# Optimization experiments

Measured on AMD Instinct MI355X. Metric: run time of the kernel, lower is better.

The kernel has to match this reference:

```python
import jax, jax.numpy as jnp
import numpy as np

N, S, T, D = 8, 2048, 2048, 1024


def setup_inputs() -> dict:
    key0 = jax.random.key(0)
    ks = jax.random.split(key0, 6)
    scale = 1.0 / np.sqrt(D).astype(np.float32)
    query = jax.random.normal(ks[0], (N, S, D), dtype=jnp.float32)
    key = jax.random.normal(ks[1], (N, T, D), dtype=jnp.float32)
    value = jax.random.normal(ks[2], (N, T, D), dtype=jnp.float32)
    # nn.Linear(D, D, bias=False) weights, shape [out, in]
    Wq = jax.random.normal(ks[3], (D, D), dtype=jnp.float32) * scale
    Wk = jax.random.normal(ks[4], (D, D), dtype=jnp.float32) * scale
    Wv = jax.random.normal(ks[5], (D, D), dtype=jnp.float32) * scale
    # causal mask: 1 on/below diagonal, 0 above (zeros become -inf additively)
    attn_mask = jnp.tril(jnp.ones((S, T), dtype=jnp.float32))
    return {"key": key, "query": query, "value": value,
            "Wq": Wq, "Wk": Wk, "Wv": Wv, "attn_mask": attn_mask}


def reference(key, query, value, Wq, Wk, Wv, attn_mask):
    d = query.shape[-1]
    q = query @ Wq.T              # [N,S,D]
    k = key @ Wk.T                # [N,T,D]
    v = value @ Wv.T              # [N,T,D]
    scores = jnp.einsum('nsd,ntd->nst', q, k)          # [N,S,T]
    # masked_fill(mask==0, -inf) then ADD the (nonzero) mask values
    additive = jnp.where(attn_mask == 0, -jnp.inf, attn_mask)
    scores = scores + additive                          # broadcast [S,T] -> [N,S,T]
    # NOTE: torch code divides by D**(-0.5), i.e. multiplies by sqrt(D). Faithful.
    attn = jax.nn.softmax(scores * jnp.sqrt(jnp.float32(d)), axis=-1)
    return jnp.einsum('nst,ntd->nsd', attn, v)          # [N,S,D]
```

## Files before the change

kernel.cpp:

```cpp
#include <hip/hip_runtime.h>
#include <hip/hip_bf16.h>


typedef __attribute__((ext_vector_type(4))) float f32x4;
typedef __attribute__((ext_vector_type(8))) short bf16x8;
typedef __attribute__((ext_vector_type(4))) short s16x4;

#define DEVI __device__ __forceinline__

DEVI unsigned short f2bf(float x) {
  union { float f; unsigned u; } v; v.f = x;
  unsigned r = v.u + 0x7FFFu + ((v.u >> 16) & 1u);
  return (unsigned short)(r >> 16);
}
DEVI float bf2f(unsigned short b) {
  union { float f; unsigned u; } v; v.u = ((unsigned)b) << 16;
  return v.f;
}

DEVI void gload16(const void* g, void* l) {
#if __has_builtin(__builtin_amdgcn_global_load_lds)
  typedef __attribute__((address_space(1))) const unsigned int* gas_u32;
  typedef __attribute__((address_space(3))) unsigned int* las_u32;
  __builtin_amdgcn_global_load_lds(
      (gas_u32)(unsigned long long)g,
      (las_u32)(unsigned int)(unsigned long long)l, 16, 0, 0);
#else
  *(bf16x8*)l = *(const bf16x8*)g;
#endif
}

DEVI int xcd_swizzle(int bid, int nwg) {
  if (nwg & 7) return bid;
  int cpx = nwg >> 3;
  return (bid & 7) * cpx + (bid >> 3);
}

#define WAITBAR(N) asm volatile("s_waitcnt vmcnt(" #N ")\ns_barrier" ::: "memory")
#define BAR()      asm volatile("s_barrier" ::: "memory")

DEVI void stage_pair(const unsigned short* __restrict__ s0, long long rs0,
                     const unsigned short* __restrict__ s1, long long rs1,
                     short* lds, int tid) {
#pragma unroll
  for (int it = 0; it < 4; ++it) {
    int ii = it * 256 + tid;
    int r = ii >> 3;
    int c8 = (ii & 7) ^ (r & 7);
    const unsigned short* src = (c8 < 4)
        ? s0 + (long long)r * rs0 + (c8 & 3) * 8
        : s1 + (long long)r * rs1 + (c8 & 3) * 8;
    gload16(src, &lds[ii * 8]);
  }
}

constexpr int NB = 8, SS = 2048, TT = 2048, DD = 1024;
constexpr long long TILE_E = 16384;

__global__ __launch_bounds__(256) void split_hl_k(
    const float* __restrict__ in, unsigned short* __restrict__ hi,
    unsigned short* __restrict__ lo, long long n4)
{
  long long i = (long long)blockIdx.x * 256 + threadIdx.x;
  long long stride = (long long)gridDim.x * 256;
  for (; i < n4; i += stride) {
    f32x4 v = ((const f32x4*)in)[i];
    s16x4 h, l;
#pragma unroll
    for (int e = 0; e < 4; ++e) {
      unsigned short hh = f2bf(v[e]);
      h[e] = (short)hh;
      l[e] = (short)f2bf(v[e] - bf2f(hh));
    }
    ((s16x4*)hi)[i] = h;
    ((s16x4*)lo)[i] = l;
  }
}

__global__ __launch_bounds__(256) void split_h_k(
    const float* __restrict__ in, unsigned short* __restrict__ hi, long long n4)
{
  long long i = (long long)blockIdx.x * 256 + threadIdx.x;
  long long stride = (long long)gridDim.x * 256;
  for (; i < n4; i += stride) {
    f32x4 v = ((const f32x4*)in)[i];
    s16x4 h;
#pragma unroll
    for (int e = 0; e < 4; ++e) h[e] = (short)f2bf(v[e]);
    ((s16x4*)hi)[i] = h;
  }
}

__global__ __launch_bounds__(256) void tsplit_k(
    const float* __restrict__ W, unsigned short* __restrict__ Th,
    unsigned short* __restrict__ Tl)
{
  __shared__ float t[64][68];
  int bi = blockIdx.x & 15, bj = blockIdx.x >> 4;
  int tid = threadIdx.x;
  int lr = tid >> 2, lc4 = tid & 3;
#pragma unroll
  for (int q = 0; q < 4; ++q) {
    int col = (lc4 + q * 4) * 4;
    f32x4 v = *(const f32x4*)(W + (long long)(bj * 64 + lr) * DD + bi * 64 + col);
    t[lr][col] = v[0]; t[lr][col + 1] = v[1];
    t[lr][col + 2] = v[2]; t[lr][col + 3] = v[3];
  }
  __syncthreads();
  int orow = tid >> 2, ch = tid & 3;
#pragma unroll
  for (int cc = 0; cc < 2; ++cc) {
    int c0 = (ch + cc * 4) * 8;
    bf16x8 h, l;
#pragma unroll
    for (int e = 0; e < 8; ++e) {
      float v = t[c0 + e][orow];
      unsigned short hh = f2bf(v);
      h[e] = (short)hh;
      l[e] = (short)f2bf(v - bf2f(hh));
    }
    long long o = (long long)(bi * 64 + orow) * DD + bj * 64 + c0;
    *(bf16x8*)(Th + o) = h;
    *(bf16x8*)(Tl + o) = l;
  }
}

template<int NMFMA, bool SPLIT_OUT>
__global__ __launch_bounds__(256, 2) void gemm_bt(
    const unsigned short* __restrict__ Ah_g, const unsigned short* __restrict__ Al_g,
    const unsigned short* __restrict__ Bh_g, const unsigned short* __restrict__ Bl_g,
    unsigned short* __restrict__ Chi, unsigned short* __restrict__ Clo,
    int Nn, int K,
    long long aStride, long long bStride, long long cStride,
    int tilesM, int tilesN)
{
  constexpr int HALF = (NMFMA == 3) ? 16384 : 8192;
  __shared__ short lds[2 * HALF];

  int tid = threadIdx.x;
  int lane = tid & 63, wid = tid >> 6;
  int wr = wid >> 1, wc = wid & 1;
  int l15 = lane & 15, lq = lane >> 4;

  int wg = xcd_swizzle(blockIdx.x, gridDim.x);
  int tilesM2 = tilesM >> 1;
  int tilesPer = tilesM2 * tilesN;
  int b = wg / tilesPer;
  int rem = wg % tilesPer;
  int mt2 = rem / tilesN, nt = rem % tilesN;

  const unsigned short* Bgh = Bh_g + (long long)b * bStride + (long long)nt * 128 * K;
  const unsigned short* Bgl = (NMFMA == 3) ? Bl_g + (long long)b * bStride + (long long)nt * 128 * K : nullptr;

  for (int hm = 0; hm < 2; ++hm) {
    int mt = mt2 + hm * tilesM2;
    const unsigned short* Agh = Ah_g + (long long)b * aStride + (long long)mt * 128 * K;
    const unsigned short* Agl = (NMFMA == 3) ? Al_g + (long long)b * aStride + (long long)mt * 128 * K : nullptr;

    f32x4 acc[4][4];
#pragma unroll
    for (int i = 0; i < 4; ++i)
#pragma unroll
      for (int j = 0; j < 4; ++j) acc[i][j] = (f32x4){0.f, 0.f, 0.f, 0.f};

    auto stage = [&](int t, int h) {
      int k0 = t * 32;
      if constexpr (NMFMA == 3) {
        stage_pair(Agh + k0, K, Agl + k0, K, lds + h * HALF, tid);
        stage_pair(Bgh + k0, K, Bgl + k0, K, lds + h * HALF + 8192, tid);
      } else {
        stage_pair(Agh + k0, K, Bgh + k0, K, lds + h * HALF, tid);
      }
    };
    auto compute = [&](int h) {
      __builtin_amdgcn_s_setprio(1);
      if constexpr (NMFMA == 3) {
        const short* U = lds + h * HALF;
        const short* V = U + 8192;
        bf16x8 afh[4], afl[4], bfh[4], bfl[4];
#pragma unroll
        for (int i = 0; i < 4; ++i) {
          int ra = wr * 64 + i * 16 + l15;
          int sa = (ra & 7) << 4;
          afh[i] = *(const bf16x8*)(&U[((ra * 128 + lq * 16) ^ sa) >> 1]);
          afl[i] = *(const bf16x8*)(&U[((ra * 128 + 64 + lq * 16) ^ sa) >> 1]);
          int rb = wc * 64 + i * 16 + l15;
          int sb = (rb & 7) << 4;
          bfh[i] = *(const bf16x8*)(&V[((rb * 128 + lq * 16) ^ sb) >> 1]);
          bfl[i] = *(const bf16x8*)(&V[((rb * 128 + 64 + lq * 16) ^ sb) >> 1]);
        }
#pragma unroll
        for (int i = 0; i < 4; ++i)
#pragma unroll
          for (int j = 0; j < 4; ++j) {
            acc[i][j] = __builtin_amdgcn_mfma_f32_16x16x32_bf16(afh[i], bfh[j], acc[i][j], 0, 0, 0);
            acc[i][j] = __builtin_amdgcn_mfma_f32_16x16x32_bf16(afh[i], bfl[j], acc[i][j], 0, 0, 0);
            acc[i][j] = __builtin_amdgcn_mfma_f32_16x16x32_bf16(afl[i], bfh[j], acc[i][j], 0, 0, 0);
          }
      } else {
        const short* W = lds + h * HALF;
        bf16x8 af[4], bfr[4];
#pragma unroll
        for (int i = 0; i < 4; ++i) {
          int ra = wr * 64 + i * 16 + l15;
          af[i] = *(const bf16x8*)(&W[((ra * 128 + lq * 16) ^ ((ra & 7) << 4)) >> 1]);
          int rb = wc * 64 + i * 16 + l15;
          bfr[i] = *(const bf16x8*)(&W[((rb * 128 + 64 + lq * 16) ^ ((rb & 7) << 4)) >> 1]);
        }
#pragma unroll
        for (int i = 0; i < 4; ++i)
#pragma unroll
          for (int j = 0; j < 4; ++j)
            acc[i][j] = __builtin_amdgcn_mfma_f32_16x16x32_bf16(af[i], bfr[j], acc[i][j], 0, 0, 0);
      }
      __builtin_amdgcn_s_setprio(0);
    };

    int NT = K >> 5;
    stage(0, 0);
    stage(1, 1);
    for (int t = 0; t < NT; ++t) {
      if (t < NT - 1) {
        if constexpr (NMFMA == 3) WAITBAR(8); else WAITBAR(4);
      } else {
        WAITBAR(0);
      }
      compute(t & 1);
      BAR();
      if (t + 2 < NT) stage(t + 2, t & 1);
    }

    unsigned short* ch = Chi + (long long)b * cStride;
    unsigned short* cl = SPLIT_OUT ? (Clo + (long long)b * cStride) : nullptr;
#pragma unroll
    for (int i = 0; i < 4; ++i)
#pragma unroll
      for (int j = 0; j < 4; ++j)
#pragma unroll
        for (int e = 0; e < 4; ++e) {
          int row = mt * 128 + wr * 64 + i * 16 + lq * 4 + e;
          int col = nt * 128 + wc * 64 + j * 16 + l15;
          float vv = acc[i][j][e];
          unsigned short h = f2bf(vv);
          ch[(long long)row * Nn + col] = h;
          if constexpr (SPLIT_OUT) cl[(long long)row * Nn + col] = f2bf(vv - bf2f(h));
        }
    BAR();
  }
}

__global__ __launch_bounds__(256, 2) void qk_bt(
    const unsigned short* __restrict__ qh, const unsigned short* __restrict__ ql,
    const unsigned short* __restrict__ kh, const unsigned short* __restrict__ kl,
    float* __restrict__ Sg)
{
  __shared__ short lds[2 * 16384];

  int tid = threadIdx.x;
  int lane = tid & 63, wid = tid >> 6;
  int wr = wid >> 1, wc = wid & 1;
  int l15 = lane & 15, lq = lane >> 4;

  int wg = xcd_swizzle(blockIdx.x, gridDim.x);
  int b = wg / 136;
  int idx = wg % 136;
  int st = (int)((sqrtf(8.f * (float)idx + 1.f) - 1.f) * 0.5f);
  while ((st + 1) * (st + 2) / 2 <= idx) ++st;
  while (st * (st + 1) / 2 > idx) --st;
  int tt = idx - st * (st + 1) / 2;

  const unsigned short* Agh = qh + (long long)b * SS * DD + (long long)st * 128 * DD;
  const unsigned short* Agl = ql + (long long)b * SS * DD + (long long)st * 128 * DD;
  const unsigned short* Bgh = kh + (long long)b * TT * DD + (long long)tt * 128 * DD;
  const unsigned short* Bgl = kl + (long long)b * TT * DD + (long long)tt * 128 * DD;

  f32x4 acc[4][4];
#pragma unroll
  for (int i = 0; i < 4; ++i)
#pragma unroll
    for (int j = 0; j < 4; ++j) acc[i][j] = (f32x4){0.f, 0.f, 0.f, 0.f};

  auto stage = [&](int t, int h) {
    int k0 = t * 32;
    stage_pair(Agh + k0, DD, Agl + k0, DD, lds + h * 16384, tid);
    stage_pair(Bgh + k0, DD, Bgl + k0, DD, lds + h * 16384 + 8192, tid);
  };
  auto compute = [&](int h) {
    __builtin_amdgcn_s_setprio(1);
    const short* U = lds + h * 16384;
    const short* V = U + 8192;
    bf16x8 afh[4], afl[4], bfh[4], bfl[4];
#pragma unroll
    for (int i = 0; i < 4; ++i) {
      int ra = wr * 64 + i * 16 + l15;
      int sa = (ra & 7) << 4;
      afh[i] = *(const bf16x8*)(&U[((ra * 128 + lq * 16) ^ sa) >> 1]);
      afl[i] = *(const bf16x8*)(&U[((ra * 128 + 64 + lq * 16) ^ sa) >> 1]);
      int rb = wc * 64 + i * 16 + l15;
      int sb = (rb & 7) << 4;
      bfh[i] = *(const bf16x8*)(&V[((rb * 128 + lq * 16) ^ sb) >> 1]);
      bfl[i] = *(const bf16x8*)(&V[((rb * 128 + 64 + lq * 16) ^ sb) >> 1]);
    }
#pragma unroll
    for (int i = 0; i < 4; ++i)
#pragma unroll
      for (int j = 0; j < 4; ++j) {
        acc[i][j] = __builtin_amdgcn_mfma_f32_16x16x32_bf16(afh[i], bfh[j], acc[i][j], 0, 0, 0);
        acc[i][j] = __builtin_amdgcn_mfma_f32_16x16x32_bf16(afh[i], bfl[j], acc[i][j], 0, 0, 0);
        acc[i][j] = __builtin_amdgcn_mfma_f32_16x16x32_bf16(afl[i], bfh[j], acc[i][j], 0, 0, 0);
      }
    __builtin_amdgcn_s_setprio(0);
  };

  stage(0, 0);
  stage(1, 1);
  for (int t = 0; t < 32; ++t) {
    if (t < 31) WAITBAR(8); else WAITBAR(0);
    compute(t & 1);
    BAR();
    if (t + 2 < 32) stage(t + 2, t & 1);
  }

  float* Sb = Sg + ((long long)b * 136 + idx) * TILE_E;
#pragma unroll
  for (int i = 0; i < 4; ++i)
#pragma unroll
    for (int j = 0; j < 4; ++j)
#pragma unroll
      for (int e = 0; e < 4; ++e) {
        int row = wr * 64 + i * 16 + lq * 4 + e;
        int col = wc * 64 + j * 16 + l15;
        Sb[(long long)row * 128 + col] = acc[i][j][e];
      }
}

__global__ __launch_bounds__(256) void softmax_kernel(float* __restrict__ Sg)
{
  __shared__ float red[8];
  int blk = blockIdx.x;
  int b = blk >> 11, s = blk & 2047;
  int st = s >> 7, r = s & 127;
  long long tri = (long long)st * (st + 1) / 2;
  const float* tb = Sg + ((long long)b * 136 + tri) * TILE_E + (long long)r * 128;

  int tid = threadIdx.x;
  int lane = tid & 63, wid = tid >> 6;

  int c0 = tid * 8;
  int tt = c0 >> 7, cc = c0 & 127;
  bool live = (c0 <= s);
  f32x4 v0 = {0.f, 0.f, 0.f, 0.f}, v1 = {0.f, 0.f, 0.f, 0.f};
  if (live) {
    const float* seg = tb + (long long)tt * TILE_E + cc;
    v0 = *(const f32x4*)seg;
    v1 = *(const f32x4*)(seg + 4);
  }

  float m = -3.0e38f;
#pragma unroll
  for (int e = 0; e < 4; ++e) {
    if (c0 + e <= s) m = fmaxf(m, v0[e]);
    if (c0 + 4 + e <= s) m = fmaxf(m, v1[e]);
  }
#pragma unroll
  for (int o = 32; o > 0; o >>= 1) m = fmaxf(m, __shfl_xor(m, o));
  if (lane == 0) red[wid] = m;
  __syncthreads();
  m = fmaxf(fmaxf(red[0], red[1]), fmaxf(red[2], red[3]));

  const float C = 46.16624130844683f;
  float p0[4], p1[4];
  float sum = 0.f;
#pragma unroll
  for (int e = 0; e < 4; ++e) {
    p0[e] = (c0 + e <= s) ? exp2f((v0[e] - m) * C) : 0.f;
    sum += p0[e];
    p1[e] = (c0 + 4 + e <= s) ? exp2f((v1[e] - m) * C) : 0.f;
    sum += p1[e];
  }
#pragma unroll
  for (int o = 32; o > 0; o >>= 1) sum += __shfl_xor(sum, o);
  if (lane == 0) red[4 + wid] = sum;
  __syncthreads();
  float inv = 1.f / (red[4] + red[5] + red[6] + red[7]);

  union { bf16x8 v; s16x4 h[2]; } w;
#pragma unroll
  for (int e = 0; e < 4; ++e) {
    w.h[0][e] = (short)f2bf(p0[e] * inv);
    w.h[1][e] = (short)f2bf(p1[e] * inv);
  }
  __syncthreads();
  if (c0 < (st + 1) * 128) {
    unsigned short* pw = (unsigned short*)Sg +
        (((long long)b * 136 + tri + tt) * TILE_E) * 2 + (long long)r * 256 + cc;
    *(bf16x8*)pw = w.v;
  }
}

__global__ __launch_bounds__(256, 2) void pv_bt(
    const unsigned short* __restrict__ P, const unsigned short* __restrict__ vT,
    float* __restrict__ Out)
{
  __shared__ short lds[2 * 8192];

  int tid = threadIdx.x;
  int lane = tid & 63, wid = tid >> 6;
  int wr = wid >> 1, wc = wid & 1;
  int l15 = lane & 15, lq = lane >> 4;

  int wg = xcd_swizzle(blockIdx.x, gridDim.x);
  int b = wg >> 7;
  int rem = wg & 127;
  int st = 15 - (rem >> 3);
  int dt = rem & 7;

  const unsigned short* Ps = P + ((long long)b * 136 + (long long)st * (st + 1) / 2) * (TILE_E * 2);
  const unsigned short* Vb = vT + (long long)b * DD * TT + (long long)dt * 128 * TT;
  int NT = (st + 1) * 4;

  f32x4 acc[4][4];
#pragma unroll
  for (int i = 0; i < 4; ++i)
#pragma unroll
    for (int j = 0; j < 4; ++j) acc[i][j] = (f32x4){0.f, 0.f, 0.f, 0.f};

  auto stage = [&](int t, int h) {
    int t0 = t * 32;
    const unsigned short* s0 = Ps + (long long)(t0 >> 7) * (TILE_E * 2) + (t0 & 127);
    stage_pair(s0, 256, Vb + t0, TT, lds + h * 8192, tid);
  };
  auto compute = [&](int h) {
    __builtin_amdgcn_s_setprio(1);
    const short* W = lds + h * 8192;
    bf16x8 af[4], bfr[4];
#pragma unroll
    for (int i = 0; i < 4; ++i) {
      int ra = wr * 64 + i * 16 + l15;
      af[i] = *(const bf16x8*)(&W[((ra * 128 + lq * 16) ^ ((ra & 7) << 4)) >> 1]);
      int rb = wc * 64 + i * 16 + l15;
      bfr[i] = *(const bf16x8*)(&W[((rb * 128 + 64 + lq * 16) ^ ((rb & 7) << 4)) >> 1]);
    }
#pragma unroll
    for (int i = 0; i < 4; ++i)
#pragma unroll
      for (int j = 0; j < 4; ++j)
        acc[i][j] = __builtin_amdgcn_mfma_f32_16x16x32_bf16(af[i], bfr[j], acc[i][j], 0, 0, 0);
    __builtin_amdgcn_s_setprio(0);
  };

  stage(0, 0);
  stage(1, 1);
  for (int t = 0; t < NT; ++t) {
    if (t < NT - 1) WAITBAR(4); else WAITBAR(0);
    compute(t & 1);
    BAR();
    if (t + 2 < NT) stage(t + 2, t & 1);
  }

  float* Ob = Out + (long long)b * SS * DD;
#pragma unroll
  for (int i = 0; i < 4; ++i)
#pragma unroll
    for (int j = 0; j < 4; ++j)
#pragma unroll
      for (int e = 0; e < 4; ++e) {
        int row = st * 128 + wr * 64 + i * 16 + lq * 4 + e;
        int col = dt * 128 + wc * 64 + j * 16 + l15;
        Ob[(long long)row * DD + col] = acc[i][j][e];
      }
}

extern "C" void kernel_launch(void* const* d_in, const int* in_sizes, int n_in,
                              void* d_out, int out_size, void* d_ws, size_t ws_size,
                              hipStream_t stream) {
  (void)in_sizes; (void)n_in; (void)out_size;
  const float* key   = (const float*)d_in[0];
  const float* query = (const float*)d_in[1];
  const float* value = (const float*)d_in[2];
  const float* Wq    = (const float*)d_in[3];
  const float* Wk    = (const float*)d_in[4];
  const float* Wv    = (const float*)d_in[5];
  float* Out = (float*)d_out;

  const long long SD = (long long)SS * DD;
  const long long DT = (long long)DD * TT;
  const long long WN = (long long)DD * DD;

  const unsigned long long PLANE_B  = (unsigned long long)SD * 2;
  const unsigned long long WPLANE_B = (unsigned long long)WN * 2;
  const unsigned long long SCORE_B  = 136ull * TILE_E * 4;

  auto need = [&](int g) -> unsigned long long {
    return 3ull * WPLANE_B + (unsigned long long)g * (SCORE_B + 5ull * PLANE_B);
  };
  int G = 1;
  for (int g : {8, 4, 2, 1}) if (ws_size >= need(g)) { G = g; break; }

  char* ws = (char*)d_ws;
  size_t off = 0;
  auto alloc = [&](unsigned long long bytes) { char* p = ws + off; off += bytes; return p; };

  unsigned short* mph = (unsigned short*)alloc(WPLANE_B);
  unsigned short* mpl = (unsigned short*)alloc(WPLANE_B);
  unsigned short* wvh = (unsigned short*)alloc(WPLANE_B);
  char* slab = alloc((unsigned long long)G * SCORE_B);
  unsigned short* qh  = (unsigned short*)alloc((unsigned long long)G * PLANE_B);
  unsigned short* ql  = (unsigned short*)alloc((unsigned long long)G * PLANE_B);
  unsigned short* kh  = (unsigned short*)alloc((unsigned long long)G * PLANE_B);
  unsigned short* kl  = (unsigned short*)alloc((unsigned long long)G * PLANE_B);
  unsigned short* vT  = (unsigned short*)alloc((unsigned long long)G * PLANE_B);

  unsigned short* wqTh = (unsigned short*)slab;
  unsigned short* wqTl = (unsigned short*)(slab + WPLANE_B);
  unsigned short* wkTh = (unsigned short*)(slab + 2 * WPLANE_B);
  unsigned short* wkTl = (unsigned short*)(slab + 3 * WPLANE_B);

  unsigned short* iah = (unsigned short*)slab;
  unsigned short* ial = (unsigned short*)(slab + (unsigned long long)G * PLANE_B);
  float* Sg = (float*)slab;

  tsplit_k<<<256, 256, 0, stream>>>(Wq, wqTh, wqTl);
  tsplit_k<<<256, 256, 0, stream>>>(Wk, wkTh, wkTl);
  split_h_k<<<512, 256, 0, stream>>>(Wv, wvh, WN / 4);
  gemm_bt<3, true><<<32, 256, 0, stream>>>(
      wkTh, wkTl, wqTh, wqTl, mph, mpl, DD, DD, 0, 0, 0, 8, 8);

  for (int b0 = 0; b0 < NB; b0 += G) {
    long long n4 = (long long)G * SD / 4;
    split_hl_k<<<2048, 256, 0, stream>>>(query + (long long)b0 * SD, iah, ial, n4);
    gemm_bt<3, true><<<G * 64, 256, 0, stream>>>(
        iah, ial, mph, mpl, qh, ql, DD, DD, SD, 0, SD, 16, 8);
    split_hl_k<<<2048, 256, 0, stream>>>(key + (long long)b0 * SD, kh, kl, n4);
    split_h_k<<<2048, 256, 0, stream>>>(value + (long long)b0 * SD, iah, n4);
    gemm_bt<1, false><<<G * 64, 256, 0, stream>>>(
        wvh, nullptr, iah, nullptr, vT, nullptr, TT, DD, 0, SD, DT, 8, 16);
    qk_bt<<<G * 136, 256, 0, stream>>>(qh, ql, kh, kl, Sg);
    softmax_kernel<<<G * SS, 256, 0, stream>>>(Sg);
    pv_bt<<<G * 128, 256, 0, stream>>>(
        (const unsigned short*)Sg, vT, Out + (long long)b0 * SD);
  }
}
```

Before: 494.5 us.

## Replace 128x128 projection GEMM with 256x256-tile, 512-thread kernel

The projection GEMM goes from a 256-thread block computing two 128x128 tiles sequentially to a 512-thread block computing one 256x256 tile. Each wave now holds an 8x4 grid of 16x16 accumulators, and the LDS double buffers double in size. The aim is more operand reuse per staged K-slice and less global and LDS traffic per MFMA. The trade-offs are higher register and LDS pressure, which may reduce occupancy, and fewer workgroups in the grid.

```diff
diff --git a/kernel.cpp b/kernel.cpp
--- a/kernel.cpp
+++ b/kernel.cpp
@@ -126,7 +126,7 @@
 }
 
 template<int NMFMA, bool SPLIT_OUT>
-__global__ __launch_bounds__(256, 2) void gemm_bt(
+__global__ __launch_bounds__(512, 2) void gemm256(
     const unsigned short* __restrict__ Ah_g, const unsigned short* __restrict__ Al_g,
     const unsigned short* __restrict__ Bh_g, const unsigned short* __restrict__ Bl_g,
     unsigned short* __restrict__ Chi, unsigned short* __restrict__ Clo,
@@ -134,119 +134,126 @@
     long long aStride, long long bStride, long long cStride,
     int tilesM, int tilesN)
 {
-  constexpr int HALF = (NMFMA == 3) ? 16384 : 8192;
+  constexpr int HALF = (NMFMA == 3) ? 32768 : 16384;
   __shared__ short lds[2 * HALF];
 
   int tid = threadIdx.x;
   int lane = tid & 63, wid = tid >> 6;
-  int wr = wid >> 1, wc = wid & 1;
+  int wr = wid >> 2, wc = wid & 3;
   int l15 = lane & 15, lq = lane >> 4;
 
   int wg = xcd_swizzle(blockIdx.x, gridDim.x);
-  int tilesM2 = tilesM >> 1;
-  int tilesPer = tilesM2 * tilesN;
+  int tilesPer = tilesM * tilesN;
   int b = wg / tilesPer;
   int rem = wg % tilesPer;
-  int mt2 = rem / tilesN, nt = rem % tilesN;
-
-  const unsigned short* Bgh = Bh_g + (long long)b * bStride + (long long)nt * 128 * K;
-  const unsigned short* Bgl = (NMFMA == 3) ? Bl_g + (long long)b * bStride + (long long)nt * 128 * K : nullptr;
-
-  for (int hm = 0; hm < 2; ++hm) {
-    int mt = mt2 + hm * tilesM2;
-    const unsigned short* Agh = Ah_g + (long long)b * aStride + (long long)mt * 128 * K;
-    const unsigned short* Agl = (NMFMA == 3) ? Al_g + (long long)b * aStride + (long long)mt * 128 * K : nullptr;
-
-    f32x4 acc[4][4];
-#pragma unroll
-    for (int i = 0; i < 4; ++i)
-#pragma unroll
-      for (int j = 0; j < 4; ++j) acc[i][j] = (f32x4){0.f, 0.f, 0.f, 0.f};
-
-    auto stage = [&](int t, int h) {
-      int k0 = t * 32;
-      if constexpr (NMFMA == 3) {
-        stage_pair(Agh + k0, K, Agl + k0, K, lds + h * HALF, tid);
-        stage_pair(Bgh + k0, K, Bgl + k0, K, lds + h * HALF + 8192, tid);
-      } else {
-        stage_pair(Agh + k0, K, Bgh + k0, K, lds + h * HALF, tid);
-      }
-    };
-    auto compute = [&](int h) {
-      __builtin_amdgcn_s_setprio(1);
-      if constexpr (NMFMA == 3) {
-        const short* U = lds + h * HALF;
-        const short* V = U + 8192;
-        bf16x8 afh[4], afl[4], bfh[4], bfl[4];
-#pragma unroll
-        for (int i = 0; i < 4; ++i) {
-          int ra = wr * 64 + i * 16 + l15;
-          int sa = (ra & 7) << 4;
-          afh[i] = *(const bf16x8*)(&U[((ra * 128 + lq * 16) ^ sa) >> 1]);
-          afl[i] = *(const bf16x8*)(&U[((ra * 128 + 64 + lq * 16) ^ sa) >> 1]);
-          int rb = wc * 64 + i * 16 + l15;
-          int sb = (rb & 7) << 4;
-          bfh[i] = *(const bf16x8*)(&V[((rb * 128 + lq * 16) ^ sb) >> 1]);
-          bfl[i] = *(const bf16x8*)(&V[((rb * 128 + 64 + lq * 16) ^ sb) >> 1]);
+  int mt = rem / tilesN, nt = rem % tilesN;
+
+  const unsigned short* Agh = Ah_g + (long long)b * aStride + (long long)mt * 256 * K;
+  const unsigned short* Bgh = Bh_g + (long long)b * bStride + (long long)nt * 256 * K;
+  const unsigned short* Agl = (NMFMA == 3) ? Al_g + (long long)b * aStride + (long long)mt * 256 * K : nullptr;
+  const unsigned short* Bgl = (NMFMA == 3) ? Bl_g + (long long)b * bStride + (long long)nt * 256 * K : nullptr;
+
+  f32x4 acc[8][4];
+#pragma unroll
+  for (int i = 0; i < 8; ++i)
+#pragma unroll
+    for (int j = 0; j < 4; ++j) acc[i][j] = (f32x4){0.f, 0.f, 0.f, 0.f};
+
+  auto stageP = [&](const unsigned short* p0, const unsigned short* p1,
+                    int k0, short* dst) {
+#pragma unroll
+    for (int it = 0; it < 4; ++it) {
+      int ii = it * 512 + tid;
+      int r = ii >> 3;
+      int c8 = (ii & 7) ^ (r & 7);
+      const unsigned short* src = ((c8 < 4) ? p0 : p1) + (long long)r * K + k0 + (c8 & 3) * 8;
+      gload16(src, &dst[ii * 8]);
+    }
+  };
+  auto stage = [&](int t, int h) {
+    int k0 = t * 32;
+    if constexpr (NMFMA == 3) {
+      stageP(Agh, Agl, k0, lds + h * HALF);
+      stageP(Bgh, Bgl, k0, lds + h * HALF + 16384);
+    } else {
+      stageP(Agh, Bgh, k0, lds + h * HALF);
+    }
+  };
+
+  auto compute = [&](int h) {
+    const short* A = lds + h * HALF;
+    __builtin_amdgcn_s_setprio(1);
+    if constexpr (NMFMA == 3) {
+      const short* B = A + 16384;
+      bf16x8 bh[4], bl[4];
+#pragma unroll
+      for (int j = 0; j < 4; ++j) {
+        int rb = wc * 64 + j * 16 + l15;
+        int sb = (rb & 7) << 4;
+        bh[j] = *(const bf16x8*)(&B[((rb * 128 + lq * 16) ^ sb) >> 1]);
+        bl[j] = *(const bf16x8*)(&B[((rb * 128 + 64 + lq * 16) ^ sb) >> 1]);
+      }
+#pragma unroll
+      for (int i = 0; i < 8; ++i) {
+        int ra = wr * 128 + i * 16 + l15;
+        int sa = (ra & 7) << 4;
+        bf16x8 ah = *(const bf16x8*)(&A[((ra * 128 + lq * 16) ^ sa) >> 1]);
+        bf16x8 al = *(const bf16x8*)(&A[((ra * 128 + 64 + lq * 16) ^ sa) >> 1]);
+#pragma unroll
+        for (int j = 0; j < 4; ++j) {
+          acc[i][j] = __builtin_amdgcn_mfma_f32_16x16x32_bf16(ah, bh[j], acc[i][j], 0, 0, 0);
+          acc[i][j] = __builtin_amdgcn_mfma_f32_16x16x32_bf16(ah, bl[j], acc[i][j], 0, 0, 0);
+          acc[i][j] = __builtin_amdgcn_mfma_f32_16x16x32_bf16(al, bh[j], acc[i][j], 0, 0, 0);
         }
-#pragma unroll
-        for (int i = 0; i < 4; ++i)
-#pragma unroll
-          for (int j = 0; j < 4; ++j) {
-            acc[i][j] = __builtin_amdgcn_mfma_f32_16x16x32_bf16(afh[i], bfh[j], acc[i][j], 0, 0, 0);
-            acc[i][j] = __builtin_amdgcn_mfma_f32_16x16x32_bf16(afh[i], bfl[j], acc[i][j], 0, 0, 0);
-            acc[i][j] = __builtin_amdgcn_mfma_f32_16x16x32_bf16(afl[i], bfh[j], acc[i][j], 0, 0, 0);
-          }
-      } else {
-        const short* W = lds + h * HALF;
-        bf16x8 af[4], bfr[4];
-#pragma unroll
-        for (int i = 0; i < 4; ++i) {
-          int ra = wr * 64 + i * 16 + l15;
-          af[i] = *(const bf16x8*)(&W[((ra * 128 + lq * 16) ^ ((ra & 7) << 4)) >> 1]);
-          int rb = wc * 64 + i * 16 + l15;
-          bfr[i] = *(const bf16x8*)(&W[((rb * 128 + 64 + lq * 16) ^ ((rb & 7) << 4)) >> 1]);
-        }
-#pragma unroll
-        for (int i = 0; i < 4; ++i)
-#pragma unroll
-          for (int j = 0; j < 4; ++j)
-            acc[i][j] = __builtin_amdgcn_mfma_f32_16x16x32_bf16(af[i], bfr[j], acc[i][j], 0, 0, 0);
-      }
-      __builtin_amdgcn_s_setprio(0);
-    };
-
-    int NT = K >> 5;
-    stage(0, 0);
-    stage(1, 1);
-    for (int t = 0; t < NT; ++t) {
-      if (t < NT - 1) {
-        if constexpr (NMFMA == 3) WAITBAR(8); else WAITBAR(4);
-      } else {
-        WAITBAR(0);
-      }
-      compute(t & 1);
-      BAR();
-      if (t + 2 < NT) stage(t + 2, t & 1);
-    }
-
-    unsigned short* ch = Chi + (long long)b * cStride;
-    unsigned short* cl = SPLIT_OUT ? (Clo + (long long)b * cStride) : nullptr;
-#pragma unroll
-    for (int i = 0; i < 4; ++i)
-#pragma unroll
-      for (int j = 0; j < 4; ++j)
-#pragma unroll
-        for (int e = 0; e < 4; ++e) {
-          int row = mt * 128 + wr * 64 + i * 16 + lq * 4 + e;
-          int col = nt * 128 + wc * 64 + j * 16 + l15;
-          float vv = acc[i][j][e];
-          unsigned short h = f2bf(vv);
-          ch[(long long)row * Nn + col] = h;
-          if constexpr (SPLIT_OUT) cl[(long long)row * Nn + col] = f2bf(vv - bf2f(h));
-        }
+      }
+    } else {
+      bf16x8 bfr[4];
+#pragma unroll
+      for (int j = 0; j < 4; ++j) {
+        int rb = wc * 64 + j * 16 + l15;
+        bfr[j] = *(const bf16x8*)(&A[((rb * 128 + 64 + lq * 16) ^ ((rb & 7) << 4)) >> 1]);
+      }
+#pragma unroll
+      for (int i = 0; i < 8; ++i) {
+        int ra = wr * 128 + i * 16 + l15;
+        bf16x8 af = *(const bf16x8*)(&A[((ra * 128 + lq * 16) ^ ((ra & 7) << 4)) >> 1]);
+#pragma unroll
+        for (int j = 0; j < 4; ++j)
+          acc[i][j] = __builtin_amdgcn_mfma_f32_16x16x32_bf16(af, bfr[j], acc[i][j], 0, 0, 0);
+      }
+    }
+    __builtin_amdgcn_s_setprio(0);
+  };
+
+  int NT = K >> 5;
+  stage(0, 0);
+  stage(1, 1);
+  for (int t = 0; t < NT; ++t) {
+    if (t < NT - 1) {
+      if constexpr (NMFMA == 3) WAITBAR(8); else WAITBAR(4);
+    } else {
+      WAITBAR(0);
+    }
+    compute(t & 1);
     BAR();
-  }
+    if (t + 2 < NT) stage(t + 2, t & 1);
+  }
+
+  unsigned short* ch = Chi + (long long)b * cStride;
+  unsigned short* cl = SPLIT_OUT ? (Clo + (long long)b * cStride) : nullptr;
+#pragma unroll
+  for (int i = 0; i < 8; ++i)
+#pragma unroll
+    for (int j = 0; j < 4; ++j)
+#pragma unroll
+      for (int e = 0; e < 4; ++e) {
+        int row = mt * 256 + wr * 128 + i * 16 + lq * 4 + e;
+        int col = nt * 256 + wc * 64 + j * 16 + l15;
+        float vv = acc[i][j][e];
+        unsigned short h = f2bf(vv);
+        ch[(long long)row * Nn + col] = h;
+        if constexpr (SPLIT_OUT) cl[(long long)row * Nn + col] = f2bf(vv - bf2f(h));
+      }
 }
 
 __global__ __launch_bounds__(256, 2) void qk_bt(
@@ -523,18 +530,18 @@
   tsplit_k<<<256, 256, 0, stream>>>(Wq, wqTh, wqTl);
   tsplit_k<<<256, 256, 0, stream>>>(Wk, wkTh, wkTl);
   split_h_k<<<512, 256, 0, stream>>>(Wv, wvh, WN / 4);
-  gemm_bt<3, true><<<32, 256, 0, stream>>>(
-      wkTh, wkTl, wqTh, wqTl, mph, mpl, DD, DD, 0, 0, 0, 8, 8);
+  gemm256<3, true><<<16, 512, 0, stream>>>(
+      wkTh, wkTl, wqTh, wqTl, mph, mpl, DD, DD, 0, 0, 0, 4, 4);
 
   for (int b0 = 0; b0 < NB; b0 += G) {
     long long n4 = (long long)G * SD / 4;
     split_hl_k<<<2048, 256, 0, stream>>>(query + (long long)b0 * SD, iah, ial, n4);
-    gemm_bt<3, true><<<G * 64, 256, 0, stream>>>(
-        iah, ial, mph, mpl, qh, ql, DD, DD, SD, 0, SD, 16, 8);
+    gemm256<3, true><<<G * 32, 512, 0, stream>>>(
+        iah, ial, mph, mpl, qh, ql, DD, DD, SD, 0, SD, 8, 4);
     split_hl_k<<<2048, 256, 0, stream>>>(key + (long long)b0 * SD, kh, kl, n4);
     split_h_k<<<2048, 256, 0, stream>>>(value + (long long)b0 * SD, iah, n4);
-    gemm_bt<1, false><<<G * 64, 256, 0, stream>>>(
-        wvh, nullptr, iah, nullptr, vT, nullptr, TT, DD, 0, SD, DT, 8, 16);
+    gemm256<1, false><<<G * 32, 512, 0, stream>>>(
+        wvh, nullptr, iah, nullptr, vT, nullptr, TT, DD, 0, SD, DT, 4, 8);
     qk_bt<<<G * 136, 256, 0, stream>>>(qh, ql, kh, kl, Sg);
     softmax_kernel<<<G * SS, 256, 0, stream>>>(Sg);
     pv_bt<<<G * 128, 256, 0, stream>>>(
```

Measured after the change: 505.5 us. 1.02x slower.

## Use 256x256-tile 8-wave split-bf16 GEMM for query projection

Applied to the files above, without the earlier changes.

Adds a new GEMM kernel with 256x256 output tiles, 512 threads (8 waves), and double-buffered LDS staging of hi/lo bf16 planes. The query projection uses it in place of the 128x128 gemm_bt. Larger tiles raise arithmetic intensity and cut redundant global loads. In exchange the kernel holds more accumulator registers and uses 128KB of LDS per block, and there are fewer blocks, which can hurt occupancy and load balance.

```diff
diff --git a/kernel.cpp b/kernel.cpp
--- a/kernel.cpp
+++ b/kernel.cpp
@@ -247,6 +247,115 @@
         }
     BAR();
   }
+}
+
+template<bool SPLIT_OUT>
+__global__ __launch_bounds__(512, 2) void gemm256p8(
+    const unsigned short* __restrict__ Ah_g, const unsigned short* __restrict__ Al_g,
+    const unsigned short* __restrict__ Bh_g, const unsigned short* __restrict__ Bl_g,
+    unsigned short* __restrict__ Chi, unsigned short* __restrict__ Clo,
+    int Nn, int K,
+    long long aStride, long long bStride, long long cStride,
+    int tilesM, int tilesN)
+{
+  __shared__ short lds[2 * 32768];
+
+  int tid = threadIdx.x;
+  int lane = tid & 63, wid = tid >> 6;
+  int wr = wid >> 2, wc = wid & 3;
+  int l15 = lane & 15, lq = lane >> 4;
+
+  int wg = xcd_swizzle(blockIdx.x, gridDim.x);
+  int tilesPer = tilesM * tilesN;
+  int b = wg / tilesPer;
+  int rem = wg % tilesPer;
+  int mt = rem / tilesN, nt = rem % tilesN;
+
+  const unsigned short* Agh = Ah_g + (long long)b * aStride + (long long)mt * 256 * K;
+  const unsigned short* Agl = Al_g + (long long)b * aStride + (long long)mt * 256 * K;
+  const unsigned short* Bgh = Bh_g + (long long)b * bStride + (long long)nt * 256 * K;
+  const unsigned short* Bgl = Bl_g + (long long)b * bStride + (long long)nt * 256 * K;
+
+  f32x4 acc[8][4];
+#pragma unroll
+  for (int i = 0; i < 8; ++i)
+#pragma unroll
+    for (int j = 0; j < 4; ++j) acc[i][j] = (f32x4){0.f, 0.f, 0.f, 0.f};
+
+  auto stageP = [&](const unsigned short* p0, const unsigned short* p1,
+                    int k0, short* dst) {
+#pragma unroll
+    for (int it = 0; it < 4; ++it) {
+      int ii = it * 512 + tid;
+      int r = ii >> 3;
+      int c8 = (ii & 7) ^ (r & 7);
+      const unsigned short* src = ((c8 < 4) ? p0 : p1) + (long long)r * K + k0 + (c8 & 3) * 8;
+      gload16(src, &dst[ii * 8]);
+    }
+  };
+  auto stage = [&](int t, int h) {
+    int k0 = t * 32;
+    stageP(Agh, Agl, k0, lds + h * 32768);
+    stageP(Bgh, Bgl, k0, lds + h * 32768 + 16384);
+  };
+
+  int NT = K >> 5;
+  stage(0, 0);
+  stage(1, 1);
+  for (int t = 0; t < NT; ++t) {
+    int h = t & 1;
+    if (t < NT - 1) WAITBAR(8); else WAITBAR(0);
+    const short* A = lds + h * 32768;
+    const short* B = A + 16384;
+#pragma unroll
+    for (int ph = 0; ph < 4; ++ph) {
+      const int ih = ph >> 1, jh = ph & 1;
+      bf16x8 bh[2], bl[2], ah[4], al[4];
+#pragma unroll
+      for (int j = 0; j < 2; ++j) {
+        int rb = wc * 64 + (jh * 2 + j) * 16 + l15;
+        int sb = (rb & 7) << 4;
+        bh[j] = *(const bf16x8*)(&B[((rb * 128 + lq * 16) ^ sb) >> 1]);
+        bl[j] = *(const bf16x8*)(&B[((rb * 128 + 64 + lq * 16) ^ sb) >> 1]);
+      }
+#pragma unroll
+      for (int i = 0; i < 4; ++i) {
+        int ra = wr * 128 + (ih * 4 + i) * 16 + l15;
+        int sa = (ra & 7) << 4;
+        ah[i] = *(const bf16x8*)(&A[((ra * 128 + lq * 16) ^ sa) >> 1]);
+        al[i] = *(const bf16x8*)(&A[((ra * 128 + 64 + lq * 16) ^ sa) >> 1]);
+      }
+      __builtin_amdgcn_s_setprio(1);
+#pragma unroll
+      for (int i = 0; i < 4; ++i)
+#pragma unroll
+        for (int j = 0; j < 2; ++j) {
+          const int I = ih * 4 + i, J = jh * 2 + j;
+          acc[I][J] = __builtin_amdgcn_mfma_f32_16x16x32_bf16(ah[i], bh[j], acc[I][J], 0, 0, 0);
+          acc[I][J] = __builtin_amdgcn_mfma_f32_16x16x32_bf16(ah[i], bl[j], acc[I][J], 0, 0, 0);
+          acc[I][J] = __builtin_amdgcn_mfma_f32_16x16x32_bf16(al[i], bh[j], acc[I][J], 0, 0, 0);
+        }
+      __builtin_amdgcn_s_setprio(0);
+      BAR();
+    }
+    if (t + 2 < NT) stage(t + 2, h);
+  }
+
+  unsigned short* ch = Chi + (long long)b * cStride;
+  unsigned short* cl = SPLIT_OUT ? (Clo + (long long)b * cStride) : nullptr;
+#pragma unroll
+  for (int i = 0; i < 8; ++i)
+#pragma unroll
+    for (int j = 0; j < 4; ++j)
+#pragma unroll
+      for (int e = 0; e < 4; ++e) {
+        int row = mt * 256 + wr * 128 + i * 16 + lq * 4 + e;
+        int col = nt * 256 + wc * 64 + j * 16 + l15;
+        float vv = acc[i][j][e];
+        unsigned short h = f2bf(vv);
+        ch[(long long)row * Nn + col] = h;
+        if constexpr (SPLIT_OUT) cl[(long long)row * Nn + col] = f2bf(vv - bf2f(h));
+      }
 }
 
 __global__ __launch_bounds__(256, 2) void qk_bt(
@@ -529,8 +638,8 @@
   for (int b0 = 0; b0 < NB; b0 += G) {
     long long n4 = (long long)G * SD / 4;
     split_hl_k<<<2048, 256, 0, stream>>>(query + (long long)b0 * SD, iah, ial, n4);
-    gemm_bt<3, true><<<G * 64, 256, 0, stream>>>(
-        iah, ial, mph, mpl, qh, ql, DD, DD, SD, 0, SD, 16, 8);
+    gemm256p8<true><<<G * 32, 512, 0, stream>>>(
+        iah, ial, mph, mpl, qh, ql, DD, DD, SD, 0, SD, 8, 4);
     split_hl_k<<<2048, 256, 0, stream>>>(key + (long long)b0 * SD, kh, kl, n4);
     split_h_k<<<2048, 256, 0, stream>>>(value + (long long)b0 * SD, iah, n4);
     gemm_bt<1, false><<<G * 64, 256, 0, stream>>>(
```

New measurement: 497.3 us. No clear change (+0.6%).
